# Kernel tuning notes

Hardware: AMD Instinct MI355X
Metric: run time of the kernel (lower is better)

The kernel has to match this reference:

```python
import jax, jax.numpy as jnp
import numpy as np
import math

B, S, C = 8, 4096, 512
WIN = 16          # window_size
G = 4             # num_global_tokens
KS = 7            # conv kernel_size
CG = C // 4       # global proj dim


def setup_inputs() -> dict:
    key = jax.random.key(0)
    ks = jax.random.split(key, 16)
    s = 1.0 / math.sqrt(C)
    sg = 1.0 / math.sqrt(CG)
    return {
        "x": jax.random.normal(ks[0], (B, S, C), dtype=jnp.float32),
        "Wq": jax.random.normal(ks[1], (C, C), dtype=jnp.float32) * s,
        "bq": jnp.zeros((C,), dtype=jnp.float32),
        "Wk": jax.random.normal(ks[2], (C, C), dtype=jnp.float32) * s,
        "bk": jnp.zeros((C,), dtype=jnp.float32),
        "Wv": jax.random.normal(ks[3], (C, C), dtype=jnp.float32) * s,
        "bv": jnp.zeros((C,), dtype=jnp.float32),
        "Wo": jax.random.normal(ks[4], (C, C), dtype=jnp.float32) * s,
        "bo": jnp.zeros((C,), dtype=jnp.float32),
        "Wg": jax.random.normal(ks[5], (C, CG), dtype=jnp.float32) * s,
        "bg": jnp.zeros((CG,), dtype=jnp.float32),
        "Wgo": jax.random.normal(ks[6], (CG, C), dtype=jnp.float32) * sg,
        "bgo": jnp.zeros((C,), dtype=jnp.float32),
        "conv_w": jax.random.normal(ks[7], (1, 2, KS), dtype=jnp.float32) * 0.2,
    }


def _forward(x, Wq, bq, Wk, bk, Wv, bv, Wo, bo, Wg, bg, Wgo, bgo, conv_w):
    b, s, c = x.shape
    q = x @ Wq + bq
    k = x @ Wk + bk
    v = x @ Wv + bv

    nw = s // WIN
    qw = q.reshape(b, nw, WIN, c)
    kw = k.reshape(b, nw, WIN, c)
    vw = v.reshape(b, nw, WIN, c)
    scale = 1.0 / math.sqrt(c)
    attn = jax.nn.softmax(jnp.einsum('bnic,bnjc->bnij', qw, kw) * scale, axis=-1)
    x_local = jnp.einsum('bnij,bnjc->bnic', attn, vw).reshape(b, s, c)

    # ---- sparse global-token attention ----
    gidx = np.linspace(0, s - 1, G).astype(np.int64)  # static indices
    gt = x[:, gidx]                       # [B,G,C]
    qg = q @ Wg + bg                      # [B,S,CG]
    kg = gt @ Wg + bg                     # [B,G,CG]
    vg = kg
    gscale = 1.0 / math.sqrt(c // 4)
    gattn = jax.nn.softmax(jnp.einsum('bsd,bgd->bsg', qg, kg) * gscale, axis=-1)
    x_global = jnp.einsum('bsg,bgd->bsd', gattn, vg) @ Wgo + bgo  # [B,S,C]

    # ---- conv gate over channel-avg / channel-max ----
    avg = jnp.mean(x, axis=2, keepdims=True)          # [B,S,1]
    mx = jnp.max(x, axis=2, keepdims=True)            # [B,S,1]
    pool = jnp.concatenate([avg, mx], axis=2)         # [B,S,2]
    pool = jnp.transpose(pool, (0, 2, 1))             # [B,2,S]
    gate = jax.lax.conv_general_dilated(
        pool, conv_w, window_strides=(1,), padding=[(KS // 2, KS // 2)],
        dimension_numbers=('NCH', 'OIH', 'NCH'))      # [B,1,S]
    gate = jax.nn.sigmoid(jnp.transpose(gate, (0, 2, 1)))  # [B,S,1]

    out = (x + x_local + x_global) * gate
    return out @ Wo + bo


def reference(x, Wq, bq, Wk, bk, Wv, bv, Wo, bo, Wg, bg, Wgo, bgo, conv_w):
    return _forward(x, Wq, bq, Wk, bk, Wv, bv, Wo, bo, Wg, bg, Wgo, bgo, conv_w)
```

## Files before the change

### kernel.cpp

```cpp
#include <hip/hip_runtime.h>
#include <hip/hip_bf16.h>

#define BB 8
#define SS 4096
#define CC 512
#define NTOK (BB*SS)
#define QKVS 1664

typedef __attribute__((ext_vector_type(8))) short bf16x8;
typedef __attribute__((ext_vector_type(4))) float f32x4;
typedef __attribute__((ext_vector_type(4))) short s16x4;

__device__ __forceinline__ float bf2f(short s) {
  return __uint_as_float(((unsigned)(unsigned short)s) << 16);
}
__device__ __forceinline__ short f2bf(float f) {
  __hip_bfloat16 h = __float2bfloat16(f);
  return *reinterpret_cast<short*>(&h);
}

__device__ __forceinline__ f32x4 pv_mfma(s16x4 a, s16x4 b, f32x4 c) {
#if __has_builtin(__builtin_amdgcn_mfma_f32_16x16x16bf16_1k)
  return __builtin_amdgcn_mfma_f32_16x16x16bf16_1k(a, b, c, 0, 0, 0);
#else
  f32x4 d;
  asm volatile("v_mfma_f32_16x16x16_bf16 %0, %1, %2, %3\n\ts_nop 7\n\ts_nop 7"
               : "=v"(d) : "v"(a), "v"(b), "v"(c));
  return d;
#endif
}

__device__ __forceinline__ void gload_lds16(const short* g, short* l) {
  __builtin_amdgcn_global_load_lds(
      (const __attribute__((address_space(1))) unsigned int*)g,
      (__attribute__((address_space(3))) unsigned int*)l, 16, 0, 0);
}

__global__ __launch_bounds__(256) void prep_weights(
    const float* __restrict__ Wq, const float* __restrict__ Wk, const float* __restrict__ Wv,
    const float* __restrict__ Wo, const float* __restrict__ Wg,
    const float* __restrict__ bq, const float* __restrict__ bk, const float* __restrict__ bv,
    const float* __restrict__ bg,
    short* __restrict__ WtQKV, short* __restrict__ WtO, short* __restrict__ WtG,
    short* __restrict__ Wqb, float* __restrict__ bqkv, float* __restrict__ zb)
{
  int i = blockIdx.x * 256 + threadIdx.x;
  if (i < 1536 * 512) {
    int n = i >> 9, k = i & 511;
    const float* W = (n < 512) ? Wq : (n < 1024) ? Wk : Wv;
    WtQKV[i] = f2bf(W[k * 512 + (n & 511)]);
  }
  if (i < 512 * 512) {
    int n = i >> 9, k = i & 511;
    WtO[i] = f2bf(Wo[k * 512 + n]);
    Wqb[i] = f2bf(Wq[i]);
  }
  if (i < 128 * 512) {
    int n = i >> 9, k = i & 511;
    WtG[i] = f2bf(Wg[k * 128 + n]);
  }
  if (i < 1536) {
    bqkv[i] = (i < 512) ? bq[i] : (i < 1024) ? bk[i - 512] : bv[i - 1024];
  }
  if (i < 512) zb[i] = 0.f;
  if (i < 128) {
    float s = bg[i];
    for (int c = 0; c < 512; c++) s += bq[c] * Wg[c * 128 + i];
    bqkv[1536 + i] = s;
  }
}

__global__ __launch_bounds__(256) void cast_pool_kernel(const float* __restrict__ x,
                                                        short* __restrict__ xb,
                                                        float* __restrict__ pavg,
                                                        float* __restrict__ pmax)
{
  int tok = blockIdx.x * 4 + (threadIdx.x >> 6);
  int lane = threadIdx.x & 63;
  const float* xr = &x[(size_t)tok * CC];
  float4 a = *(const float4*)&xr[lane * 4];
  float4 b = *(const float4*)&xr[256 + lane * 4];
  s16x4 oa, ob;
  oa[0] = f2bf(a.x); oa[1] = f2bf(a.y); oa[2] = f2bf(a.z); oa[3] = f2bf(a.w);
  ob[0] = f2bf(b.x); ob[1] = f2bf(b.y); ob[2] = f2bf(b.z); ob[3] = f2bf(b.w);
  *(s16x4*)&xb[(size_t)tok * CC + lane * 4] = oa;
  *(s16x4*)&xb[(size_t)tok * CC + 256 + lane * 4] = ob;
  float s = (a.x + a.y) + (a.z + a.w) + (b.x + b.y) + (b.z + b.w);
  float m = fmaxf(fmaxf(fmaxf(a.x, a.y), fmaxf(a.z, a.w)),
                  fmaxf(fmaxf(b.x, b.y), fmaxf(b.z, b.w)));
#pragma unroll
  for (int off = 32; off; off >>= 1) {
    s += __shfl_down(s, off);
    m = fmaxf(m, __shfl_down(m, off));
  }
  if (lane == 0) { pavg[tok] = s * (1.0f / CC); pmax[tok] = m; }
}

template<int OUT_BF16, int SWZ>
__global__ __launch_bounds__(256, 2) void gemm_kernel(
    const short* __restrict__ A,
    const short* __restrict__ Wt,
    const float* __restrict__ bias,
    void* __restrict__ Cp, int ldc, int nx)
{
  __shared__ short As0[128 * 64], As1[128 * 64];
  __shared__ short Bs0[128 * 64], Bs1[128 * 64];
  int id = blockIdx.x;
  if (SWZ) {
    const int cpx = gridDim.x >> 3;
    id = (id & 7) * cpx + (id >> 3);
  }
  const int n0 = (id % nx) * 128;
  const int m0 = (id / nx) * 128;
  const int t = threadIdx.x;
  const int lane = t & 63, w = t >> 6;
  const int wm = (w >> 1) * 64, wn = (w & 1) * 64;
  const int lr = lane & 15;
  const int g8b = (lane >> 4) * 16;
  const int xorb = (lr & 7) << 4;

  const int srow = w * 8 + (lane >> 3);
  const int scol = (((lane & 7) ^ (lane >> 3)) << 4) >> 1;
  const short* Ag = A + (size_t)(m0 + srow) * 512 + scol;
  const short* Bg = Wt + (size_t)(n0 + srow) * 512 + scol;
  const int sloff = (w * 8) * 64;

  f32x4 acc[4][4];
#pragma unroll
  for (int i = 0; i < 4; i++)
#pragma unroll
    for (int j = 0; j < 4; j++) acc[i][j] = (f32x4){0.f, 0.f, 0.f, 0.f};

#define STAGE(AL, BL, KOFF)                                          \
  do {                                                               \
    _Pragma("unroll")                                                \
    for (int s_ = 0; s_ < 4; s_++) {                                 \
      gload_lds16(Ag + (KOFF) + s_ * (32 * 512), &AL[sloff + s_ * (32 * 64)]); \
      gload_lds16(Bg + (KOFF) + s_ * (32 * 512), &BL[sloff + s_ * (32 * 64)]); \
    }                                                                \
  } while (0)

#define COMPUTE(AL, BL)                                                           \
  do {                                                                            \
    _Pragma("unroll")                                                             \
    for (int kk = 0; kk < 2; kk++) {                                              \
      bf16x8 af[4], bfr[4];                                                       \
      const int ko = ((kk * 64 + g8b) ^ xorb) >> 1;                               \
      _Pragma("unroll")                                                           \
      for (int mt = 0; mt < 4; mt++) af[mt]  = *(bf16x8*)&AL[(wm + mt * 16 + lr) * 64 + ko]; \
      _Pragma("unroll")                                                           \
      for (int nt = 0; nt < 4; nt++) bfr[nt] = *(bf16x8*)&BL[(wn + nt * 16 + lr) * 64 + ko]; \
      _Pragma("unroll")                                                           \
      for (int mt = 0; mt < 4; mt++)                                              \
        _Pragma("unroll")                                                         \
        for (int nt = 0; nt < 4; nt++)                                            \
          acc[mt][nt] = __builtin_amdgcn_mfma_f32_16x16x32_bf16(af[mt], bfr[nt], acc[mt][nt], 0, 0, 0); \
    }                                                                             \
  } while (0)

  STAGE(As0, Bs0, 0);
  __syncthreads();
#pragma unroll
  for (int tt = 0; tt < 3; tt++) {
    STAGE(As1, Bs1, tt * 128 + 64);
    COMPUTE(As0, Bs0);
    __syncthreads();
    STAGE(As0, Bs0, tt * 128 + 128);
    COMPUTE(As1, Bs1);
    __syncthreads();
  }
  STAGE(As1, Bs1, 448);
  COMPUTE(As0, Bs0);
  __syncthreads();
  COMPUTE(As1, Bs1);
#undef STAGE
#undef COMPUTE

  const int cr = (lane >> 4) * 4;
#pragma unroll
  for (int nt = 0; nt < 4; nt++) {
    int col = n0 + wn + nt * 16 + lr;
    float bv = bias[col];
#pragma unroll
    for (int mt = 0; mt < 4; mt++) {
      int row = m0 + wm + mt * 16 + cr;
#pragma unroll
      for (int j = 0; j < 4; j++) {
        float v = acc[mt][nt][j] + bv;
        if (OUT_BF16) ((short*)Cp)[(size_t)(row + j) * ldc + col] = f2bf(v);
        else          ((float*)Cp)[(size_t)(row + j) * ldc + col] = v;
      }
    }
  }
}

__global__ __launch_bounds__(256, 4) void winattn_combine_kernel(
    const short* __restrict__ qkvb, const short* __restrict__ xb,
    const float* __restrict__ kg, const float* __restrict__ kgo,
    const float* __restrict__ bgo, const float* __restrict__ pavg,
    const float* __restrict__ pmax, const float* __restrict__ conv_w,
    short* __restrict__ y)
{
  __shared__ short vs[2][16][512];
  __shared__ float scs[32][4];
  __shared__ float4 esm[32];
  __shared__ float gateb[32];
  const int t = threadIdx.x;
  const int lane = t & 63, w = t >> 6;
  const int t0b = blockIdx.x * 32;
  const int bb = t0b >> 12;
  const int win = w >> 1, half = w & 1;
  const int t0 = t0b + win * 16;

  {
    const int rb = half * 8;
#pragma unroll
    for (int i = 0; i < 8; i++) {
      const int r = rb + i;
      const short* vrow = &qkvb[(size_t)(t0 + r) * QKVS + 1024];
      gload_lds16(vrow + ((lane ^ (r & 7)) << 3), &vs[win][r][0]);
    }
  }

  if (t < 128) {
    const int tl = t >> 2, gi = t & 3;
    const short* qr = &qkvb[(size_t)(t0b + tl) * QKVS + 1536];
    const float* kr = &kg[bb * 512 + gi * 128];
    float s = 0.f;
    for (int d0 = 0; d0 < 128; d0 += 8) {
      bf16x8 qv = *(const bf16x8*)&qr[d0];
#pragma unroll
      for (int u = 0; u < 8; u++) s += bf2f(qv[u]) * kr[d0 + u];
    }
    scs[tl][gi] = s * 0.08838834764831845f;
  }
  __syncthreads();
  if (t < 32) {
    float p0 = scs[t][0], p1 = scs[t][1], p2 = scs[t][2], p3 = scs[t][3];
    float mx = fmaxf(fmaxf(p0, p1), fmaxf(p2, p3));
    float e0 = __expf(p0 - mx), e1 = __expf(p1 - mx), e2 = __expf(p2 - mx), e3 = __expf(p3 - mx);
    float inv = 1.0f / (e0 + e1 + e2 + e3);
    esm[t] = make_float4(e0 * inv, e1 * inv, e2 * inv, e3 * inv);
    int s = (t0b + t) & 4095;
    float g = 0.f;
#pragma unroll
    for (int tk = 0; tk < 7; tk++) {
      int ss = s + tk - 3;
      if (ss >= 0 && ss < SS)
        g += conv_w[tk] * pavg[bb * SS + ss] + conv_w[7 + tk] * pmax[bb * SS + ss];
    }
    gateb[t] = 1.0f / (1.0f + __expf(-g));
  }

  const int qrow = lane & 15;
  const int grp8 = (lane >> 4) * 8;
  const int krow = (lane >> 4) * 4;
  const int colo = lane & 15;

  const short* kqbase = &qkvb[(size_t)(t0 + qrow) * QKVS];
  f32x4 accA = (f32x4){0.f, 0.f, 0.f, 0.f};
  f32x4 accB = (f32x4){0.f, 0.f, 0.f, 0.f};
#pragma unroll
  for (int k0 = 0; k0 < 512; k0 += 64) {
    bf16x8 kf0 = *(const bf16x8*)&kqbase[512 + k0 + grp8];
    bf16x8 qf0 = *(const bf16x8*)&kqbase[k0 + grp8];
    bf16x8 kf1 = *(const bf16x8*)&kqbase[512 + k0 + 32 + grp8];
    bf16x8 qf1 = *(const bf16x8*)&kqbase[k0 + 32 + grp8];
    accA = __builtin_amdgcn_mfma_f32_16x16x32_bf16(kf0, qf0, accA, 0, 0, 0);
    accB = __builtin_amdgcn_mfma_f32_16x16x32_bf16(kf1, qf1, accB, 0, 0, 0);
  }

  const float scale = 0.04419417382415922f;
  float s0 = (accA[0] + accB[0]) * scale, s1 = (accA[1] + accB[1]) * scale;
  float s2 = (accA[2] + accB[2]) * scale, s3 = (accA[3] + accB[3]) * scale;
  float m = fmaxf(fmaxf(s0, s1), fmaxf(s2, s3));
  m = fmaxf(m, __shfl_xor(m, 16));
  m = fmaxf(m, __shfl_xor(m, 32));
  float e0 = __expf(s0 - m), e1 = __expf(s1 - m), e2 = __expf(s2 - m), e3 = __expf(s3 - m);
  float sum = e0 + e1 + e2 + e3;
  sum += __shfl_xor(sum, 16);
  sum += __shfl_xor(sum, 32);
  float inv = 1.0f / sum;
  s16x4 pa;
  pa[0] = f2bf(e0 * inv); pa[1] = f2bf(e1 * inv);
  pa[2] = f2bf(e2 * inv); pa[3] = f2bf(e3 * inv);

#pragma unroll
  for (int ct = 0; ct < 16; ct++) {
    const int cb = (half * 256 + ct * 16 + colo) * 2;
    s16x4 bf;
#pragma unroll
    for (int u = 0; u < 4; u++) {
      const int r = krow + u;
      bf[u] = vs[win][r][(cb ^ ((r & 7) << 4)) >> 1];
    }
    f32x4 d = pv_mfma(pa, bf, (f32x4){0.f, 0.f, 0.f, 0.f});
#pragma unroll
    for (int jj = 0; jj < 4; jj++) {
      const int r = krow + jj;
      vs[win][r][(cb ^ ((r & 7) << 4)) >> 1] = f2bf(d[jj]);
    }
  }
  __syncthreads();

  const int r = t >> 3;
  const int rowg = t0b + r;
  const int winr = r >> 4, rr = r & 15;
  const float4 e = esm[r];
  const float g = gateb[r];
  const float* kgr = &kgo[bb * 2048];
  const short* xrow = &xb[(size_t)rowg * CC];
  const short* xlrow = &vs[winr][rr][0];
  short* yrow = &y[(size_t)rowg * CC];
#pragma unroll
  for (int it = 0; it < 8; it++) {
    const int c = (t & 7) * 8 + it * 64;
    bf16x8 xv  = *(const bf16x8*)&xrow[c];
    bf16x8 xlv = *(const bf16x8*)&xlrow[((c * 2) ^ ((rr & 7) << 4)) >> 1];
    float4 k0a = *(const float4*)&kgr[c],        k0b = *(const float4*)&kgr[c + 4];
    float4 k1a = *(const float4*)&kgr[512 + c],  k1b = *(const float4*)&kgr[512 + c + 4];
    float4 k2a = *(const float4*)&kgr[1024 + c], k2b = *(const float4*)&kgr[1024 + c + 4];
    float4 k3a = *(const float4*)&kgr[1536 + c], k3b = *(const float4*)&kgr[1536 + c + 4];
    float4 ba  = *(const float4*)&bgo[c],        bbv = *(const float4*)&bgo[c + 4];
    float xg[8];
    xg[0] = e.x * k0a.x + e.y * k1a.x + e.z * k2a.x + e.w * k3a.x + ba.x;
    xg[1] = e.x * k0a.y + e.y * k1a.y + e.z * k2a.y + e.w * k3a.y + ba.y;
    xg[2] = e.x * k0a.z + e.y * k1a.z + e.z * k2a.z + e.w * k3a.z + ba.z;
    xg[3] = e.x * k0a.w + e.y * k1a.w + e.z * k2a.w + e.w * k3a.w + ba.w;
    xg[4] = e.x * k0b.x + e.y * k1b.x + e.z * k2b.x + e.w * k3b.x + bbv.x;
    xg[5] = e.x * k0b.y + e.y * k1b.y + e.z * k2b.y + e.w * k3b.y + bbv.y;
    xg[6] = e.x * k0b.z + e.y * k1b.z + e.z * k2b.z + e.w * k3b.z + bbv.z;
    xg[7] = e.x * k0b.w + e.y * k1b.w + e.z * k2b.w + e.w * k3b.w + bbv.w;
    bf16x8 ov;
#pragma unroll
    for (int u = 0; u < 8; u++)
      ov[u] = f2bf((bf2f(xv[u]) + bf2f(xlv[u]) + xg[u]) * g);
    *(bf16x8*)&yrow[c] = ov;
  }
}

__global__ __launch_bounds__(256) void kg_kgo_kernel(const float* __restrict__ x,
                                                     const float* __restrict__ Wg,
                                                     const float* __restrict__ bg,
                                                     const float* __restrict__ Wgo,
                                                     float* __restrict__ kg,
                                                     float* __restrict__ kgo)
{
  __shared__ float kr[128];
  const int bg_ = blockIdx.x;
  const int b = bg_ >> 2, g = bg_ & 3;
  const int gidx[4] = {0, 1365, 2730, 4095};
  const int t = threadIdx.x;
  const float* xr = &x[((size_t)b * SS + gidx[g]) * CC];
  if (t < 128) {
    float s = bg[t];
    for (int c = 0; c < CC; c++) s += xr[c] * Wg[c * 128 + t];
    kr[t] = s;
    kg[bg_ * 128 + t] = s;
  }
  __syncthreads();
  for (int c = t; c < 512; c += 256) {
    float s = 0.f;
    for (int d = 0; d < 128; d++) s += kr[d] * Wgo[d * 512 + c];
    kgo[bg_ * 512 + c] = s;
  }
}

extern "C" void kernel_launch(void* const* d_in, const int* in_sizes, int n_in,
                              void* d_out, int out_size, void* d_ws, size_t ws_size,
                              hipStream_t stream)
{
  const float* x     = (const float*)d_in[0];
  const float* Wq    = (const float*)d_in[1];
  const float* bq    = (const float*)d_in[2];
  const float* Wk    = (const float*)d_in[3];
  const float* bk    = (const float*)d_in[4];
  const float* Wv    = (const float*)d_in[5];
  const float* bv    = (const float*)d_in[6];
  const float* Wo    = (const float*)d_in[7];
  const float* bo    = (const float*)d_in[8];
  const float* Wg    = (const float*)d_in[9];
  const float* bg    = (const float*)d_in[10];
  const float* Wgo   = (const float*)d_in[11];
  const float* bgo   = (const float*)d_in[12];
  const float* convw = (const float*)d_in[13];
  float* out = (float*)d_out;

  char* ws = (char*)d_ws;
  size_t off = 0;
  auto alloc = [&](size_t bytes) -> void* {
    void* p = ws + off;
    off += (bytes + 255) & ~(size_t)255;
    return p;
  };
  short* xb    = (short*)alloc((size_t)NTOK * CC * 2);
  short* qkvb  = (short*)alloc((size_t)NTOK * QKVS * 2);
  short* WtQKV = (short*)alloc((size_t)QKVS * 512 * 2);
  short* WtO   = (short*)alloc((size_t)512 * 512 * 2);
  short* WtG   = (short*)alloc((size_t)128 * 512 * 2);
  short* Wqb   = (short*)alloc((size_t)512 * 512 * 2);
  float* bqkv  = (float*)alloc(QKVS * 4);
  float* zb    = (float*)alloc(512 * 4);
  float* kg    = (float*)alloc(8 * 4 * 128 * 4);
  float* kgo   = (float*)alloc(8 * 4 * 512 * 4);
  float* pavg  = (float*)alloc((size_t)NTOK * 4);
  float* pmax  = (float*)alloc((size_t)NTOK * 4);
  short* ybuf  = (short*)alloc((size_t)NTOK * CC * 2);
  short* WtQG  = WtQKV + (size_t)1536 * 512;

  prep_weights<<<3072, 256, 0, stream>>>(Wq, Wk, Wv, Wo, Wg, bq, bk, bv, bg,
                                         WtQKV, WtO, WtG, Wqb, bqkv, zb);
  cast_pool_kernel<<<NTOK / 4, 256, 0, stream>>>(x, xb, pavg, pmax);
  kg_kgo_kernel<<<32, 256, 0, stream>>>(x, Wg, bg, Wgo, kg, kgo);

  gemm_kernel<1, 0><<<4, 256, 0, stream>>>(WtG, Wqb, zb, WtQG, 512, 4);

  gemm_kernel<1, 1><<<13 * 256, 256, 0, stream>>>(xb, WtQKV, bqkv, qkvb, QKVS, 13);

  winattn_combine_kernel<<<NTOK / 32, 256, 0, stream>>>(qkvb, xb, kg, kgo, bgo,
                                                        pavg, pmax, convw, ybuf);

  gemm_kernel<0, 1><<<4 * 256, 256, 0, stream>>>(ybuf, WtO, bo, out, CC, 4);
}
```

Baseline: 213.2 us.

## Triple-buffer GEMM K-loop with 32-wide tiles and parallelize global-token scoring

The GEMM main loop changes from a double-buffered 64-wide K tile to a triple-buffered 32-wide K tile. Two stages are kept in flight using vmcnt waits and raw barriers, and launch bounds rise to three blocks per CU since shared memory per block shrinks. In the window-attention kernel, the global-token score computation moves from 128 threads doing serial 128-long dot products to all 256 threads, with eight lanes per token and a shuffle reduction. It is placed after the QK MFMA loop, which removes one early __syncthreads. The risks are more barriers per K step in the GEMM, higher register pressure at three blocks per CU, and a new swizzle that must stay correct.

```diff
diff --git a/kernel.cpp b/kernel.cpp
--- a/kernel.cpp
+++ b/kernel.cpp
@@ -97,14 +97,14 @@
 }
 
 template<int OUT_BF16, int SWZ>
-__global__ __launch_bounds__(256, 2) void gemm_kernel(
+__global__ __launch_bounds__(256, 3) void gemm_kernel(
     const short* __restrict__ A,
     const short* __restrict__ Wt,
     const float* __restrict__ bias,
     void* __restrict__ Cp, int ldc, int nx)
 {
-  __shared__ short As0[128 * 64], As1[128 * 64];
-  __shared__ short Bs0[128 * 64], Bs1[128 * 64];
+  __shared__ short As[3][128 * 32];
+  __shared__ short Bs[3][128 * 32];
   int id = blockIdx.x;
   if (SWZ) {
     const int cpx = gridDim.x >> 3;
@@ -116,14 +116,15 @@
   const int lane = t & 63, w = t >> 6;
   const int wm = (w >> 1) * 64, wn = (w & 1) * 64;
   const int lr = lane & 15;
-  const int g8b = (lane >> 4) * 16;
-  const int xorb = (lr & 7) << 4;
-
-  const int srow = w * 8 + (lane >> 3);
-  const int scol = (((lane & 7) ^ (lane >> 3)) << 4) >> 1;
-  const short* Ag = A + (size_t)(m0 + srow) * 512 + scol;
-  const short* Bg = Wt + (size_t)(n0 + srow) * 512 + scol;
-  const int sloff = (w * 8) * 64;
+  const int koff = (((lane >> 4) ^ ((lr >> 1) & 3)) << 3);
+
+  const int srow = w * 16 + (lane >> 2);
+  const int scol = (((lane & 3) ^ ((lane >> 3) & 3)) << 3);
+  const short* Ag0 = A + (size_t)(m0 + srow) * 512 + scol;
+  const short* Ag1 = Ag0 + (size_t)64 * 512;
+  const short* Bg0 = Wt + (size_t)(n0 + srow) * 512 + scol;
+  const short* Bg1 = Bg0 + (size_t)64 * 512;
+  const int l0 = (w * 16) * 32, l1 = (64 + w * 16) * 32;
 
   f32x4 acc[4][4];
 #pragma unroll
@@ -131,48 +132,38 @@
 #pragma unroll
     for (int j = 0; j < 4; j++) acc[i][j] = (f32x4){0.f, 0.f, 0.f, 0.f};
 
-#define STAGE(AL, BL, KOFF)                                          \
-  do {                                                               \
-    _Pragma("unroll")                                                \
-    for (int s_ = 0; s_ < 4; s_++) {                                 \
-      gload_lds16(Ag + (KOFF) + s_ * (32 * 512), &AL[sloff + s_ * (32 * 64)]); \
-      gload_lds16(Bg + (KOFF) + s_ * (32 * 512), &BL[sloff + s_ * (32 * 64)]); \
-    }                                                                \
+#define STAGE(B_, KO)                                  \
+  do {                                                 \
+    gload_lds16(Ag0 + (KO), &As[B_][l0]);              \
+    gload_lds16(Ag1 + (KO), &As[B_][l1]);              \
+    gload_lds16(Bg0 + (KO), &Bs[B_][l0]);              \
+    gload_lds16(Bg1 + (KO), &Bs[B_][l1]);              \
   } while (0)
 
-#define COMPUTE(AL, BL)                                                           \
+#define COMPUTE(B_)                                                               \
   do {                                                                            \
+    bf16x8 af[4], bfr[4];                                                         \
     _Pragma("unroll")                                                             \
-    for (int kk = 0; kk < 2; kk++) {                                              \
-      bf16x8 af[4], bfr[4];                                                       \
-      const int ko = ((kk * 64 + g8b) ^ xorb) >> 1;                               \
+    for (int mt = 0; mt < 4; mt++) af[mt]  = *(bf16x8*)&As[B_][(wm + mt * 16 + lr) * 32 + koff]; \
+    _Pragma("unroll")                                                             \
+    for (int nt = 0; nt < 4; nt++) bfr[nt] = *(bf16x8*)&Bs[B_][(wn + nt * 16 + lr) * 32 + koff]; \
+    _Pragma("unroll")                                                             \
+    for (int mt = 0; mt < 4; mt++)                                                \
       _Pragma("unroll")                                                           \
-      for (int mt = 0; mt < 4; mt++) af[mt]  = *(bf16x8*)&AL[(wm + mt * 16 + lr) * 64 + ko]; \
-      _Pragma("unroll")                                                           \
-      for (int nt = 0; nt < 4; nt++) bfr[nt] = *(bf16x8*)&BL[(wn + nt * 16 + lr) * 64 + ko]; \
-      _Pragma("unroll")                                                           \
-      for (int mt = 0; mt < 4; mt++)                                              \
-        _Pragma("unroll")                                                         \
-        for (int nt = 0; nt < 4; nt++)                                            \
-          acc[mt][nt] = __builtin_amdgcn_mfma_f32_16x16x32_bf16(af[mt], bfr[nt], acc[mt][nt], 0, 0, 0); \
-    }                                                                             \
+      for (int nt = 0; nt < 4; nt++)                                              \
+        acc[mt][nt] = __builtin_amdgcn_mfma_f32_16x16x32_bf16(af[mt], bfr[nt], acc[mt][nt], 0, 0, 0); \
   } while (0)
 
-  STAGE(As0, Bs0, 0);
-  __syncthreads();
-#pragma unroll
-  for (int tt = 0; tt < 3; tt++) {
-    STAGE(As1, Bs1, tt * 128 + 64);
-    COMPUTE(As0, Bs0);
-    __syncthreads();
-    STAGE(As0, Bs0, tt * 128 + 128);
-    COMPUTE(As1, Bs1);
-    __syncthreads();
-  }
-  STAGE(As1, Bs1, 448);
-  COMPUTE(As0, Bs0);
-  __syncthreads();
-  COMPUTE(As1, Bs1);
+  STAGE(0, 0);
+  STAGE(1, 32);
+#pragma unroll
+  for (int tt = 0; tt < 16; tt++) {
+    if (tt == 15) asm volatile("s_waitcnt vmcnt(0)" ::: "memory");
+    else          asm volatile("s_waitcnt vmcnt(4)" ::: "memory");
+    __builtin_amdgcn_s_barrier();
+    if (tt < 14) STAGE((tt + 2) % 3, (tt + 2) * 32);
+    COMPUTE(tt % 3);
+  }
 #undef STAGE
 #undef COMPUTE
 
@@ -202,7 +193,6 @@
     short* __restrict__ y)
 {
   __shared__ short vs[2][16][512];
-  __shared__ float scs[32][4];
   __shared__ float4 esm[32];
   __shared__ float gateb[32];
   const int t = threadIdx.x;
@@ -222,36 +212,6 @@
     }
   }
 
-  if (t < 128) {
-    const int tl = t >> 2, gi = t & 3;
-    const short* qr = &qkvb[(size_t)(t0b + tl) * QKVS + 1536];
-    const float* kr = &kg[bb * 512 + gi * 128];
-    float s = 0.f;
-    for (int d0 = 0; d0 < 128; d0 += 8) {
-      bf16x8 qv = *(const bf16x8*)&qr[d0];
-#pragma unroll
-      for (int u = 0; u < 8; u++) s += bf2f(qv[u]) * kr[d0 + u];
-    }
-    scs[tl][gi] = s * 0.08838834764831845f;
-  }
-  __syncthreads();
-  if (t < 32) {
-    float p0 = scs[t][0], p1 = scs[t][1], p2 = scs[t][2], p3 = scs[t][3];
-    float mx = fmaxf(fmaxf(p0, p1), fmaxf(p2, p3));
-    float e0 = __expf(p0 - mx), e1 = __expf(p1 - mx), e2 = __expf(p2 - mx), e3 = __expf(p3 - mx);
-    float inv = 1.0f / (e0 + e1 + e2 + e3);
-    esm[t] = make_float4(e0 * inv, e1 * inv, e2 * inv, e3 * inv);
-    int s = (t0b + t) & 4095;
-    float g = 0.f;
-#pragma unroll
-    for (int tk = 0; tk < 7; tk++) {
-      int ss = s + tk - 3;
-      if (ss >= 0 && ss < SS)
-        g += conv_w[tk] * pavg[bb * SS + ss] + conv_w[7 + tk] * pmax[bb * SS + ss];
-    }
-    gateb[t] = 1.0f / (1.0f + __expf(-g));
-  }
-
   const int qrow = lane & 15;
   const int grp8 = (lane >> 4) * 8;
   const int krow = (lane >> 4) * 4;
@@ -268,6 +228,50 @@
     bf16x8 qf1 = *(const bf16x8*)&kqbase[k0 + 32 + grp8];
     accA = __builtin_amdgcn_mfma_f32_16x16x32_bf16(kf0, qf0, accA, 0, 0, 0);
     accB = __builtin_amdgcn_mfma_f32_16x16x32_bf16(kf1, qf1, accB, 0, 0, 0);
+  }
+
+  {
+    const int tl = w * 8 + (lane >> 3);
+    const int sub = lane & 7;
+    const short* qr = &qkvb[(size_t)(t0b + tl) * QKVS + 1536 + sub * 16];
+    bf16x8 qv0 = *(const bf16x8*)&qr[0];
+    bf16x8 qv1 = *(const bf16x8*)&qr[8];
+    const float* kr = &kg[bb * 512 + sub * 16];
+    float p[4];
+#pragma unroll
+    for (int g = 0; g < 4; g++) {
+      float4 ka = *(const float4*)&kr[g * 128];
+      float4 kbv = *(const float4*)&kr[g * 128 + 4];
+      float4 kc = *(const float4*)&kr[g * 128 + 8];
+      float4 kd = *(const float4*)&kr[g * 128 + 12];
+      float s = bf2f(qv0[0]) * ka.x + bf2f(qv0[1]) * ka.y + bf2f(qv0[2]) * ka.z + bf2f(qv0[3]) * ka.w
+              + bf2f(qv0[4]) * kbv.x + bf2f(qv0[5]) * kbv.y + bf2f(qv0[6]) * kbv.z + bf2f(qv0[7]) * kbv.w
+              + bf2f(qv1[0]) * kc.x + bf2f(qv1[1]) * kc.y + bf2f(qv1[2]) * kc.z + bf2f(qv1[3]) * kc.w
+              + bf2f(qv1[4]) * kd.x + bf2f(qv1[5]) * kd.y + bf2f(qv1[6]) * kd.z + bf2f(qv1[7]) * kd.w;
+      p[g] = s;
+    }
+#pragma unroll
+    for (int off = 1; off < 8; off <<= 1) {
+#pragma unroll
+      for (int g = 0; g < 4; g++) p[g] += __shfl_xor(p[g], off);
+    }
+    if (sub == 0) {
+      const float gs = 0.08838834764831845f;
+      float p0 = p[0] * gs, p1 = p[1] * gs, p2 = p[2] * gs, p3 = p[3] * gs;
+      float mx = fmaxf(fmaxf(p0, p1), fmaxf(p2, p3));
+      float e0 = __expf(p0 - mx), e1 = __expf(p1 - mx), e2 = __expf(p2 - mx), e3 = __expf(p3 - mx);
+      float inv = 1.0f / (e0 + e1 + e2 + e3);
+      esm[tl] = make_float4(e0 * inv, e1 * inv, e2 * inv, e3 * inv);
+      int s = (t0b + tl) & 4095;
+      float g = 0.f;
+#pragma unroll
+      for (int tk = 0; tk < 7; tk++) {
+        int ss = s + tk - 3;
+        if (ss >= 0 && ss < SS)
+          g += conv_w[tk] * pavg[bb * SS + ss] + conv_w[7 + tk] * pmax[bb * SS + ss];
+      }
+      gateb[tl] = 1.0f / (1.0f + __expf(-g));
+    }
   }
 
   const float scale = 0.04419417382415922f;
@@ -284,6 +288,8 @@
   s16x4 pa;
   pa[0] = f2bf(e0 * inv); pa[1] = f2bf(e1 * inv);
   pa[2] = f2bf(e2 * inv); pa[3] = f2bf(e3 * inv);
+
+  __syncthreads();
 
 #pragma unroll
   for (int ct = 0; ct < 16; ct++) {
```

Result: slower. 221.3 us (+3.8%).
